# Kernel optimization log

Measured on AMD Instinct MI355X. Metric: run time of the kernel, lower is better.

The kernel has to match this reference:

```python
import jax, jax.numpy as jnp
import numpy as np

N_COM = 40000
N_POS = 40000
E = 1000000
D = 128


def setup_inputs() -> dict:
    key = jax.random.key(0)
    ks = jax.random.split(key, 20)
    def idx(k, n):
        return jax.random.randint(k, (E,), 0, n)
    inp = {
        "com_emb": jax.random.normal(ks[0], (N_COM, D), jnp.float32),
        "pos_emb": jax.random.normal(ks[1], (N_POS, D), jnp.float32),
        # Demand: company -> position
        "demand_src": idx(ks[2], N_COM), "demand_dst": idx(ks[3], N_POS),
        "demand_w": jax.random.uniform(ks[4], (E,), jnp.float32),
        # Supply: position -> company
        "supply_src": idx(ks[5], N_POS), "supply_dst": idx(ks[6], N_COM),
        "supply_w": jax.random.uniform(ks[7], (E,), jnp.float32),
        # CompanyFlow: company -> company
        "cflow_src": idx(ks[8], N_COM), "cflow_dst": idx(ks[9], N_COM),
        "cflow_w": jax.random.uniform(ks[10], (E,), jnp.float32),
        # PositionFlow: position -> position
        "pflow_src": idx(ks[11], N_POS), "pflow_dst": idx(ks[12], N_POS),
        "pflow_w": jax.random.uniform(ks[13], (E,), jnp.float32),
    }
    s = float(1.0 / np.sqrt(D))
    for i, name in enumerate(["demand", "supply", "cflow", "pflow"]):
        inp[f"W_{name}"] = jax.random.uniform(ks[14 + i], (D, D), jnp.float32, -s, s)
        inp[f"b_{name}"] = jnp.zeros((D,), jnp.float32)
    return inp


def _graph_conv(h_src, src, dst, w, W, b, n_src, n_dst):
    # dgl EdgeWeightNorm(norm='both') on the relation subgraph:
    # w_norm = w / sqrt(weighted_out_deg(src) * weighted_in_deg(dst))
    deg_out = jax.ops.segment_sum(w, src, num_segments=n_src)  # [n_src]
    deg_in = jax.ops.segment_sum(w, dst, num_segments=n_dst)   # [n_dst]
    wn = w * jax.lax.rsqrt(deg_out[src] * deg_in[dst])         # [E]
    # dgl GraphConv(norm='none'): project first (in==out feats), then
    # weighted gather/scatter-sum aggregation, bias, ReLU activation.
    msg = (h_src @ W)[src] * wn[:, None]                       # [E, D]
    agg = jax.ops.segment_sum(msg, dst, num_segments=n_dst)    # [n_dst, D]
    return jax.nn.relu(agg + b)


def reference(com_emb, pos_emb,
              demand_src, demand_dst, demand_w,
              supply_src, supply_dst, supply_w,
              cflow_src, cflow_dst, cflow_w,
              pflow_src, pflow_dst, pflow_w,
              W_demand, b_demand, W_supply, b_supply,
              W_cflow, b_cflow, W_pflow, b_pflow):
    demand = _graph_conv(com_emb, demand_src, demand_dst, demand_w, W_demand, b_demand, N_COM, N_POS)
    pflow = _graph_conv(pos_emb, pflow_src, pflow_dst, pflow_w, W_pflow, b_pflow, N_POS, N_POS)
    supply = _graph_conv(pos_emb, supply_src, supply_dst, supply_w, W_supply, b_supply, N_POS, N_COM)
    cflow = _graph_conv(com_emb, cflow_src, cflow_dst, cflow_w, W_cflow, b_cflow, N_COM, N_COM)
    # HeteroGraphConv aggregate='mean' over relations per destination ntype
    com_out = 0.5 * (supply + cflow)   # [N_COM, D]
    pos_out = 0.5 * (demand + pflow)   # [N_POS, D]
    return jnp.stack([com_out, pos_out])  # [2, N, D] (stacked ntype dict)
```

## Files before the change

### kernel.cpp

```cpp
#include <hip/hip_runtime.h>
#include <hip/hip_fp16.h>

#define D   128
#define NN  40000
#define NB  625
#define GS  64

typedef unsigned long long ull;
typedef __attribute__((ext_vector_type(8))) _Float16 f16x8;
typedef __attribute__((ext_vector_type(4))) float f32x4;

struct Ptrs { const int* src[4]; const int* dst[4]; const float* w[4]; };

__global__ __launch_bounds__(256) void conv_kernel(
    const float* __restrict__ in, __half* __restrict__ out, int n8)
{
    int i = blockIdx.x * 256 + threadIdx.x;
    if (i >= n8) return;
    const float4* a = (const float4*)in + (size_t)i * 2;
    float4 v0 = a[0], v1 = a[1];
    __half2 pack[4];
    pack[0] = __floats2half2_rn(v0.x, v0.y);
    pack[1] = __floats2half2_rn(v0.z, v0.w);
    pack[2] = __floats2half2_rn(v1.x, v1.y);
    pack[3] = __floats2half2_rn(v1.z, v1.w);
    ((float4*)out)[i] = *(float4*)pack;
}

__global__ __launch_bounds__(256) void wpack_kernel(
    const float* __restrict__ W0, const float* __restrict__ W1,
    const float* __restrict__ W2, const float* __restrict__ W3,
    __half* __restrict__ wp)
{
    int t = blockIdx.x * 256 + threadIdx.x;
    int rel = t >> 11;
    int idx = t & 2047;
    int lane = idx & 63;
    int ct = (idx >> 6) & 7;
    int kt = idx >> 9;
    const float* W = rel == 0 ? W0 : rel == 1 ? W1 : rel == 2 ? W2 : W3;
    int k0 = kt * 32 + (lane >> 4) * 8;
    int col = ct * 16 + (lane & 15);
    __half tmp[8];
#pragma unroll
    for (int j = 0; j < 8; ++j)
        tmp[j] = __float2half_rn(W[(size_t)(k0 + j) * D + col]);
    *(float4*)(wp + (size_t)t * 8) = *(float4*)tmp;
}

__global__ __launch_bounds__(1024) void hist_kernel(
    Ptrs p, __half* __restrict__ histo16, int* __restrict__ cnt_store, int E)
{
    __shared__ float hist[NN];
    __shared__ int cnt[NB];
    const int bx  = blockIdx.x;
    const int rel = bx >> 6;
    const int rep = bx & (GS - 1);
    const int tid = threadIdx.x;

    for (int i = tid; i < NN; i += 1024) hist[i] = 0.f;
    for (int i = tid; i < NB; i += 1024) cnt[i] = 0;
    __syncthreads();

    const int es  = (E + GS - 1) / GS;
    const int beg = rep * es;
    const int end = min(beg + es, E);
    const int* srcp = p.src[rel];
    const int* dstp = p.dst[rel];
    const float* w = p.w[rel];
    for (int e = beg + tid; e < end; e += 1024) {
        atomicAdd(&hist[srcp[e]], w[e]);
        atomicAdd(&cnt[dstp[e] >> 6], 1);
    }
    __syncthreads();

    __half2* outp = (__half2*)(histo16 + (size_t)bx * NN);
    for (int i = tid; i < NN / 2; i += 1024)
        outp[i] = __floats2half2_rn(hist[2 * i], hist[2 * i + 1]);
    for (int b = tid; b < NB; b += 1024)
        cnt_store[((size_t)(rel * NB + b)) * GS + rep] = cnt[b];
}

__global__ __launch_bounds__(256) void reduce_kernel(
    const __half* __restrict__ histo16, float* __restrict__ rdego, int total)
{
    int i = blockIdx.x * 256 + threadIdx.x;
    if (i >= total) return;
    int rel = i / NN;
    int node = i - rel * NN;
    const __half* bp = histo16 + (size_t)rel * GS * NN + node;
    float v = 0.f;
#pragma unroll
    for (int r = 0; r < GS; ++r) v += __half2float(bp[(size_t)r * NN]);
    rdego[i] = rsqrtf(v);
}

__device__ inline int block_excl_scan(int v, int tid) {
    __shared__ int wsum[16];
    int lane = tid & 63, wid = tid >> 6;
    int x = v;
#pragma unroll
    for (int off = 1; off < 64; off <<= 1) {
        int y = __shfl_up(x, off, 64);
        if (lane >= off) x += y;
    }
    if (lane == 63) wsum[wid] = x;
    __syncthreads();
    if (wid == 0) {
        int y = (lane < 16) ? wsum[lane] : 0;
#pragma unroll
        for (int off = 1; off < 16; off <<= 1) {
            int t = __shfl_up(y, off, 64);
            if (lane >= off) y += t;
        }
        if (lane < 16) wsum[lane] = y;
    }
    __syncthreads();
    int woff = wid ? wsum[wid - 1] : 0;
    return woff + x - v;
}

__global__ __launch_bounds__(1024) void scan1_kernel(
    const int* __restrict__ cnt_store, int* __restrict__ scanex,
    int* __restrict__ bsum, int total)
{
    int tid = threadIdx.x;
    int i = blockIdx.x * 1024 + tid;
    int v = (i < total) ? cnt_store[i] : 0;
    int excl = block_excl_scan(v, tid);
    if (i < total) scanex[i] = excl;
    if (tid == 1023) bsum[blockIdx.x] = excl + v;
}

__global__ __launch_bounds__(1024) void scan2_kernel(int* __restrict__ bsum, int nb)
{
    int tid = threadIdx.x;
    int v = (tid < nb) ? bsum[tid] : 0;
    int excl = block_excl_scan(v, tid);
    if (tid < nb) bsum[tid] = excl;
}

__global__ __launch_bounds__(256) void scan3_kernel(
    const int* __restrict__ scanex, const int* __restrict__ bsum,
    int* __restrict__ cursor_base, int* __restrict__ bucket_ptr,
    int total, int E)
{
    int i = blockIdx.x * 256 + threadIdx.x;
    if (i >= total) return;
    int v = scanex[i] + bsum[i >> 10];
    int rel = i / (NB * GS);
    int rem = i - rel * (NB * GS);
    int b = rem / GS, rep = rem - b * GS;
    int local = v - rel * E;
    cursor_base[i] = local;
    if (rep == 0) bucket_ptr[rel * (NB + 1) + b] = local;
    if (rem == 0) bucket_ptr[rel * (NB + 1) + NB] = E;
}

__global__ __launch_bounds__(512) void fill4_kernel(
    Ptrs p, const int* __restrict__ cursor_base,
    ull* __restrict__ csr8, int E)
{
    __shared__ int lcur[NB];
    const int rel = blockIdx.x / GS;
    const int rep = blockIdx.x - rel * GS;
    const int tid = threadIdx.x;
    const int* cb = cursor_base + (size_t)rel * NB * GS;
    for (int b = tid; b < NB; b += 512)
        lcur[b] = cb[(size_t)b * GS + rep];
    __syncthreads();
    const int es  = (E + GS - 1) / GS;
    const int beg = rep * es;
    const int end = min(beg + es, E);
    const int* src = p.src[rel];
    const int* dst = p.dst[rel];
    const float* w = p.w[rel];
    ull* c8 = csr8 + (size_t)rel * E;
    for (int e = beg + tid; e < end; e += 512) {
        int s = src[e];
        int d = dst[e];
        int pos = atomicAdd(&lcur[d >> 6], 1);
        ull rec = (ull)(unsigned)(s | ((d & 63) << 16)) |
                  ((ull)__float_as_uint(w[e]) << 32);
        c8[pos] = rec;
    }
}

__global__ __launch_bounds__(256) void sort24_kernel(
    const int* __restrict__ bucket_ptr, const ull* __restrict__ csr8,
    const float* __restrict__ rdego, unsigned* __restrict__ csr2u,
    int* __restrict__ row_ptr, int E)
{
    __shared__ int cnt[64];
    __shared__ int cur[64];
    __shared__ float swsum[64];
    const int rel = blockIdx.x / NB;
    const int b   = blockIdx.x - rel * NB;
    const int tid = threadIdx.x;
    const int* bp_r = bucket_ptr + rel * (NB + 1);
    const ull* c8 = csr8 + (size_t)rel * E;
    unsigned* c2 = csr2u + (size_t)rel * E;
    int* rp_r = row_ptr + rel * (NN + 1);
    const float* rd = rdego + (size_t)rel * NN;
    const int beg = bp_r[b];
    const int end = bp_r[b + 1];
    if (tid < 64) { cnt[tid] = 0; swsum[tid] = 0.f; }
    __syncthreads();
    for (int e = beg + tid; e < end; e += 256) {
        ull rec = c8[e];
        int j = (int)((rec >> 16) & 63);
        atomicAdd(&cnt[j], 1);
        atomicAdd(&swsum[j], __uint_as_float((unsigned)(rec >> 32)));
    }
    __syncthreads();
    if (tid < 64) {
        int v = cnt[tid];
        int x = v;
#pragma unroll
        for (int off = 1; off < 64; off <<= 1) {
            int y = __shfl_up(x, off, 64);
            if (tid >= off) x += y;
        }
        int start = beg + x - v;
        cur[tid] = start;
        rp_r[b * 64 + tid] = start;
        swsum[tid] = rsqrtf(swsum[tid]);
        if (b == 0 && tid == 0) rp_r[NN] = E;
    }
    __syncthreads();
    for (int e = beg + tid; e < end; e += 256) {
        ull rec = c8[e];
        int j = (int)((rec >> 16) & 63);
        int s = (int)(rec & 0xFFFF);
        float wn = __uint_as_float((unsigned)(rec >> 32)) * rd[s] * swsum[j];
        int pos = atomicAdd(&cur[j], 1);
        c2[pos] = (unsigned)s |
                  ((unsigned)__half_as_ushort(__float2half_rn(wn)) << 16);
    }
}

__global__ __launch_bounds__(256) void gather4_kernel(
    const int* __restrict__ row_ptr, const unsigned* __restrict__ csr2u,
    const __half* __restrict__ h16com, const __half* __restrict__ h16pos,
    __half* __restrict__ agg16, int gBlocks, int E)
{
    int rel = blockIdx.x / gBlocks;
    int lb  = blockIdx.x - rel * gBlocks;
    int node = (lb * 256 + threadIdx.x) >> 6;
    int lane = threadIdx.x & 63;
    if (node >= NN) return;
    const int* rp = row_ptr + rel * (NN + 1);
    const unsigned* c2 = csr2u + (size_t)rel * E;
    const __half* h16 = (rel == 0 || rel == 3) ? h16com : h16pos;
    __half* agg = agg16 + (size_t)rel * NN * D;

    int beg = rp[node], end = rp[node + 1];
    const int g = lane >> 4, l16 = lane & 15;

    float acc[8] = {};
    int e = beg;
    for (; e + 8 <= end; e += 8) {
        unsigned rec0 = __builtin_nontemporal_load(c2 + e + g);
        unsigned rec1 = __builtin_nontemporal_load(c2 + e + 4 + g);
        int s0 = (int)(rec0 & 0xFFFF);
        int s1 = (int)(rec1 & 0xFFFF);
        f32x4 hv0 = ((const f32x4*)(h16 + (size_t)s0 * D))[l16];
        f32x4 hv1 = ((const f32x4*)(h16 + (size_t)s1 * D))[l16];
        float wn0 = __half2float(__ushort_as_half((unsigned short)(rec0 >> 16)));
        float wn1 = __half2float(__ushort_as_half((unsigned short)(rec1 >> 16)));
        __half2* hp0 = (__half2*)&hv0;
        __half2* hp1 = (__half2*)&hv1;
#pragma unroll
        for (int k = 0; k < 4; ++k) {
            float2 f0 = __half22float2(hp0[k]);
            float2 f1 = __half22float2(hp1[k]);
            acc[2 * k]     += wn0 * f0.x + wn1 * f1.x;
            acc[2 * k + 1] += wn0 * f0.y + wn1 * f1.y;
        }
    }
    for (; e < end; e += 4) {
        int ee = e + g;
        int valid = ee < end;
        unsigned rec = __builtin_nontemporal_load(c2 + (valid ? ee : (end - 1)));
        int s = (int)(rec & 0xFFFF);
        float wn = valid ? __half2float(__ushort_as_half((unsigned short)(rec >> 16))) : 0.f;
        f32x4 hv4 = ((const f32x4*)(h16 + (size_t)s * D))[l16];
        __half2* hp = (__half2*)&hv4;
#pragma unroll
        for (int k = 0; k < 4; ++k) {
            float2 f = __half22float2(hp[k]);
            acc[2 * k]     += wn * f.x;
            acc[2 * k + 1] += wn * f.y;
        }
    }
#pragma unroll
    for (int k = 0; k < 8; ++k) {
        acc[k] += __shfl_xor(acc[k], 16, 64);
        acc[k] += __shfl_xor(acc[k], 32, 64);
    }
    if (g == 0) {
        __half2 pack[4];
        pack[0] = __floats2half2_rn(acc[0], acc[1]);
        pack[1] = __floats2half2_rn(acc[2], acc[3]);
        pack[2] = __floats2half2_rn(acc[4], acc[5]);
        pack[3] = __floats2half2_rn(acc[6], acc[7]);
        __builtin_nontemporal_store(*(f32x4*)pack,
                                    (f32x4*)(agg + (size_t)node * D) + l16);
    }
}

__global__ __launch_bounds__(256) void projmf_kernel(
    const __half* __restrict__ aggA, const __half* __restrict__ wpA,
    const float* __restrict__ bA,
    const __half* __restrict__ aggB, const __half* __restrict__ wpB,
    const float* __restrict__ bB, float* __restrict__ outh)
{
    __shared__ char As[2][64 * 256];
    const int t = threadIdx.x;
    const int row0 = blockIdx.x * 64;

    for (int r2 = 0; r2 < 2; ++r2) {
        const float4* src = (const float4*)((r2 ? aggB : aggA) + (size_t)row0 * D);
        for (int i = t; i < 1024; i += 256) {
            int row = i >> 4, ch = i & 15;
            int byte = row * 256 + ch * 16;
            byte ^= (row & 7) << 4;
            *(float4*)(As[r2] + byte) = src[i];
        }
    }
    __syncthreads();

    const int wv = t >> 6, lane = t & 63;
    const int rbase = wv * 16;

    f16x8 aA[4], aB[4];
#pragma unroll
    for (int kt = 0; kt < 4; ++kt) {
        int row = rbase + (lane & 15);
        int byte = row * 256 + kt * 64 + (lane >> 4) * 16;
        byte ^= (row & 7) << 4;
        aA[kt] = *(const f16x8*)(As[0] + byte);
        aB[kt] = *(const f16x8*)(As[1] + byte);
    }

    f32x4 accA[8], accB[8];
#pragma unroll
    for (int i = 0; i < 8; ++i) {
        accA[i] = (f32x4){0.f, 0.f, 0.f, 0.f};
        accB[i] = (f32x4){0.f, 0.f, 0.f, 0.f};
    }

#pragma unroll
    for (int ct = 0; ct < 8; ++ct) {
#pragma unroll
        for (int kt = 0; kt < 4; ++kt) {
            f16x8 bfA = *(const f16x8*)(wpA + ((size_t)((kt * 8 + ct) * 64 + lane)) * 8);
            f16x8 bfB = *(const f16x8*)(wpB + ((size_t)((kt * 8 + ct) * 64 + lane)) * 8);
            accA[ct] = __builtin_amdgcn_mfma_f32_16x16x32_f16(aA[kt], bfA, accA[ct], 0, 0, 0);
            accB[ct] = __builtin_amdgcn_mfma_f32_16x16x32_f16(aB[kt], bfB, accB[ct], 0, 0, 0);
        }
    }

#pragma unroll
    for (int ct = 0; ct < 8; ++ct) {
        int col = ct * 16 + (lane & 15);
        float ba = bA[col], bb = bB[col];
#pragma unroll
        for (int v = 0; v < 4; ++v) {
            int row = row0 + rbase + (lane >> 4) * 4 + v;
            float r = 0.5f * (fmaxf(accA[ct][v] + ba, 0.f) +
                              fmaxf(accB[ct][v] + bb, 0.f));
            outh[(size_t)row * D + col] = r;
        }
    }
}

extern "C" void kernel_launch(void* const* d_in, const int* in_sizes, int n_in,
                              void* d_out, int out_size, void* d_ws, size_t ws_size,
                              hipStream_t stream) {
    const float* com_emb = (const float*)d_in[0];
    const float* pos_emb = (const float*)d_in[1];
    const int E = in_sizes[2];
    const int N = NN;

    float* out = (float*)d_out;
    float* out_com = out;
    float* out_pos = out + (size_t)N * D;

    Ptrs ptrs;
    ptrs.src[0] = (const int*)d_in[8];  ptrs.dst[0] = (const int*)d_in[9];  ptrs.w[0] = (const float*)d_in[10];
    ptrs.src[1] = (const int*)d_in[5];  ptrs.dst[1] = (const int*)d_in[6];  ptrs.w[1] = (const float*)d_in[7];
    ptrs.src[2] = (const int*)d_in[11]; ptrs.dst[2] = (const int*)d_in[12]; ptrs.w[2] = (const float*)d_in[13];
    ptrs.src[3] = (const int*)d_in[2];  ptrs.dst[3] = (const int*)d_in[3];  ptrs.w[3] = (const float*)d_in[4];

    const int totalCnt = 4 * NB * GS;
    char* p = (char*)d_ws;
    float* rdego       = (float*)p;  p += (size_t)4 * N * 4;
    int*   cnt_store   = (int*)p;    p += (size_t)totalCnt * 4;
    int*   scanex      = (int*)p;    p += (size_t)totalCnt * 4;
    int*   bsum        = (int*)p;    p += (size_t)1024 * 4;
    int*   cursor_base = (int*)p;    p += (size_t)totalCnt * 4;
    int*   bucket_ptr  = (int*)p;    p += (size_t)4 * (NB + 1) * 4;
    int*   row_ptr     = (int*)p;    p += (size_t)4 * (N + 1) * 4;
    ull*   csr8        = (ull*)p;    p += (size_t)4 * E * 8;
    unsigned* csr2u    = (unsigned*)p; p += (size_t)4 * E * 4;
    __half* h16com     = (__half*)p; p += (size_t)N * D * 2;
    __half* h16pos     = (__half*)p; p += (size_t)N * D * 2;
    __half* agg16      = (__half*)p; p += (size_t)4 * N * D * 2;
    __half* wpack      = (__half*)p; p += (size_t)4 * 2048 * 8 * 2;
    __half* histo16    = (__half*)p;

    const int cBlocks = (N * D / 8 + 255) / 256;
    const int gBlocks = N / 4;
    const int sBlocks = (totalCnt + 1023) / 1024;

    conv_kernel<<<cBlocks, 256, 0, stream>>>(com_emb, h16com, N * D / 8);
    conv_kernel<<<cBlocks, 256, 0, stream>>>(pos_emb, h16pos, N * D / 8);
    wpack_kernel<<<32, 256, 0, stream>>>((const float*)d_in[18], (const float*)d_in[16],
                                         (const float*)d_in[20], (const float*)d_in[14],
                                         wpack);

    hist_kernel<<<4 * GS, 1024, 0, stream>>>(ptrs, histo16, cnt_store, E);
    reduce_kernel<<<(4 * N + 255) / 256, 256, 0, stream>>>(histo16, rdego, 4 * N);
    scan1_kernel<<<sBlocks, 1024, 0, stream>>>(cnt_store, scanex, bsum, totalCnt);
    scan2_kernel<<<1, 1024, 0, stream>>>(bsum, sBlocks);
    scan3_kernel<<<(totalCnt + 255) / 256, 256, 0, stream>>>(scanex, bsum, cursor_base,
                                                             bucket_ptr, totalCnt, E);

    fill4_kernel<<<4 * GS, 512, 0, stream>>>(ptrs, cursor_base, csr8, E);
    sort24_kernel<<<4 * NB, 256, 0, stream>>>(bucket_ptr, csr8, rdego, csr2u, row_ptr, E);
    gather4_kernel<<<4 * gBlocks, 256, 0, stream>>>(row_ptr, csr2u, h16com, h16pos,
                                                    agg16, gBlocks, E);

    projmf_kernel<<<N / 64, 256, 0, stream>>>(
        agg16 + (size_t)1 * N * D, wpack + (size_t)1 * 16384, (const float*)d_in[17],
        agg16 + (size_t)0 * N * D, wpack + (size_t)0 * 16384, (const float*)d_in[19],
        out_com);
    projmf_kernel<<<N / 64, 256, 0, stream>>>(
        agg16 + (size_t)3 * N * D, wpack + (size_t)3 * 16384, (const float*)d_in[15],
        agg16 + (size_t)2 * N * D, wpack + (size_t)2 * 16384, (const float*)d_in[21],
        out_pos);
}
```

Baseline: 310.2 us.

## Cache bucket records in LDS for sort pass and unroll gather to 16 edges

The sort kernel now stages up to SCAP bucket records in shared memory during the counting pass, so the second scatter pass reads them from LDS instead of reloading them from global memory. The gather kernel's main loop processes 16 edges per iteration (four independent row loads per lane group), where it previously handled 8. The aim is more memory-level parallelism for the random feature-row gathers. The costs are 32KB of LDS per sort block, which may lower occupancy, and higher register pressure in the gather loop.

Measured after the change: 319.3 us. 1.03x slower.

```diff
diff --git a/kernel.cpp b/kernel.cpp
--- a/kernel.cpp
+++ b/kernel.cpp
@@ -5,6 +5,7 @@
 #define NN  40000
 #define NB  625
 #define GS  64
+#define SCAP 4096
 
 typedef unsigned long long ull;
 typedef __attribute__((ext_vector_type(8))) _Float16 f16x8;
@@ -191,6 +192,7 @@
     const float* __restrict__ rdego, unsigned* __restrict__ csr2u,
     int* __restrict__ row_ptr, int E)
 {
+    __shared__ ull recs[SCAP];
     __shared__ int cnt[64];
     __shared__ int cur[64];
     __shared__ float swsum[64];
@@ -208,6 +210,8 @@
     __syncthreads();
     for (int e = beg + tid; e < end; e += 256) {
         ull rec = c8[e];
+        int idx = e - beg;
+        if (idx < SCAP) recs[idx] = rec;
         int j = (int)((rec >> 16) & 63);
         atomicAdd(&cnt[j], 1);
         atomicAdd(&swsum[j], __uint_as_float((unsigned)(rec >> 32)));
@@ -229,7 +233,8 @@
     }
     __syncthreads();
     for (int e = beg + tid; e < end; e += 256) {
-        ull rec = c8[e];
+        int idx = e - beg;
+        ull rec = (idx < SCAP) ? recs[idx] : c8[e];
         int j = (int)((rec >> 16) & 63);
         int s = (int)(rec & 0xFFFF);
         float wn = __uint_as_float((unsigned)(rec >> 32)) * rd[s] * swsum[j];
@@ -259,23 +264,25 @@
 
     float acc[8] = {};
     int e = beg;
-    for (; e + 8 <= end; e += 8) {
-        unsigned rec0 = __builtin_nontemporal_load(c2 + e + g);
-        unsigned rec1 = __builtin_nontemporal_load(c2 + e + 4 + g);
-        int s0 = (int)(rec0 & 0xFFFF);
-        int s1 = (int)(rec1 & 0xFFFF);
-        f32x4 hv0 = ((const f32x4*)(h16 + (size_t)s0 * D))[l16];
-        f32x4 hv1 = ((const f32x4*)(h16 + (size_t)s1 * D))[l16];
-        float wn0 = __half2float(__ushort_as_half((unsigned short)(rec0 >> 16)));
-        float wn1 = __half2float(__ushort_as_half((unsigned short)(rec1 >> 16)));
-        __half2* hp0 = (__half2*)&hv0;
-        __half2* hp1 = (__half2*)&hv1;
-#pragma unroll
-        for (int k = 0; k < 4; ++k) {
-            float2 f0 = __half22float2(hp0[k]);
-            float2 f1 = __half22float2(hp1[k]);
-            acc[2 * k]     += wn0 * f0.x + wn1 * f1.x;
-            acc[2 * k + 1] += wn0 * f0.y + wn1 * f1.y;
+    for (; e + 16 <= end; e += 16) {
+        unsigned rc[4];
+#pragma unroll
+        for (int d4 = 0; d4 < 4; ++d4)
+            rc[d4] = __builtin_nontemporal_load(c2 + e + 4 * d4 + g);
+        f32x4 hv[4];
+#pragma unroll
+        for (int d4 = 0; d4 < 4; ++d4)
+            hv[d4] = ((const f32x4*)(h16 + (size_t)(rc[d4] & 0xFFFF) * D))[l16];
+#pragma unroll
+        for (int d4 = 0; d4 < 4; ++d4) {
+            float wn = __half2float(__ushort_as_half((unsigned short)(rc[d4] >> 16)));
+            __half2* hp = (__half2*)&hv[d4];
+#pragma unroll
+            for (int k = 0; k < 4; ++k) {
+                float2 f = __half22float2(hp[k]);
+                acc[2 * k]     += wn * f.x;
+                acc[2 * k + 1] += wn * f.y;
+            }
         }
     }
     for (; e < end; e += 4) {
```
